# Kernel optimization log

Hardware: AMD Instinct MI355X
Metric: run time of the kernel (lower is better)

Reference implementation:

```python
import jax, jax.numpy as jnp
import numpy as np

B, T, D, H, STRIDE, MLP = 2, 2048, 1024, 16, 8, 4096
HD = D // H
EPS = 1e-5


def _ln(x, g, b):
    m = x.mean(-1, keepdims=True)
    v = x.var(-1, keepdims=True)
    return (x - m) * jax.lax.rsqrt(v + EPS) * g + b


def setup_inputs() -> dict:
    key = jax.random.key(0)
    ks = jax.random.split(key, 6)
    s = lambda k, shape: (jax.random.normal(k, shape, jnp.float32) * 0.02)
    return {
        "x": jax.random.normal(ks[0], (B, T, D), jnp.float32),
        "w_in": s(ks[1], (3 * D, D)),   # torch in_proj_weight
        "b_in": jnp.zeros((3 * D,), jnp.float32),
        "w_out": s(ks[2], (D, D)),      # attn out_proj
        "b_out": jnp.zeros((D,), jnp.float32),
        "w1": s(ks[3], (MLP, D)),       # mlp first Linear (torch layout [out,in])
        "b1": jnp.zeros((MLP,), jnp.float32),
        "w2": s(ks[4], (D, MLP)),       # mlp second Linear
        "b2": jnp.zeros((D,), jnp.float32),
        "ln1_g": jnp.ones((D,), jnp.float32),
        "ln1_b": jnp.zeros((D,), jnp.float32),
        "ln2_g": jnp.ones((D,), jnp.float32),
        "ln2_b": jnp.zeros((D,), jnp.float32),
    }


def reference(x, w_in, b_in, w_out, b_out, w1, b1, w2, b2,
              ln1_g, ln1_b, ln2_g, ln2_b):
    Bs, Ts, Ds = x.shape
    xn = _ln(x, ln1_g, ln1_b)
    # fused qkv projection (torch Linear: y = x @ W.T + b)
    qkv = xn @ w_in.T + b_in                              # [B,T,3D]
    q, k, v = jnp.split(qkv, 3, axis=-1)
    to_heads = lambda t: t.reshape(Bs, Ts, H, HD).transpose(0, 2, 1, 3)
    q, k, v = to_heads(q), to_heads(k), to_heads(v)       # [B,H,T,hd]
    scores = jnp.einsum("bhqd,bhkd->bhqk", q, k) / jnp.sqrt(jnp.float32(HD))
    # mask: rows at multiples of STRIDE attend everywhere; others only to self
    idx = jnp.arange(Ts)
    allowed = ((idx % STRIDE) == 0)[:, None] | (idx[:, None] == idx[None, :])
    scores = jnp.where(allowed, scores, -jnp.inf)
    attn = jax.nn.softmax(scores, axis=-1)
    o = jnp.einsum("bhqk,bhkd->bhqd", attn, v)            # [B,H,T,hd]
    o = o.transpose(0, 2, 1, 3).reshape(Bs, Ts, Ds)
    o = o @ w_out.T + b_out
    x = x + o
    xn = _ln(x, ln2_g, ln2_b)
    h = jax.nn.gelu(xn @ w1.T + b1, approximate=False)    # torch nn.GELU default = exact
    x = x + (h @ w2.T + b2)
    return x
```

## Files before the change

### kernel.cpp

```cpp
#include <hip/hip_runtime.h>

#define D_ 1024
#define T_ 2048
#define B_ 2
#define H_ 16
#define MLP_ 4096
#define NTOK (B_*T_)
#define QG 256
#define L2E 1.44269504088896340736f

typedef float f32x4 __attribute__((ext_vector_type(4)));
typedef __bf16 bf16x8 __attribute__((ext_vector_type(8)));

__device__ __forceinline__ unsigned short f2bf(float f) {
  unsigned int u = __float_as_uint(f);
  u += 0x7fff + ((u >> 16) & 1);
  return (unsigned short)(u >> 16);
}

__device__ __forceinline__ float wave_sum(float v) {
  for (int o = 32; o > 0; o >>= 1) v += __shfl_down(v, o, 64);
  return v;
}

__device__ __forceinline__ void gload16(const unsigned short* g, unsigned short* l) {
  __builtin_amdgcn_global_load_lds(
      (const __attribute__((address_space(1))) void*)g,
      (__attribute__((address_space(3))) void*)l, 16, 0, 0);
}

#define N4_WIN  786432
#define N4_WOUT 262144
#define N4_W1   1048576
#define N4_W2   1048576
__global__ void cast_all_kernel(const float* __restrict__ w_in,
                                const float* __restrict__ w_out,
                                const float* __restrict__ w1,
                                const float* __restrict__ w2,
                                unsigned short* __restrict__ o_in,
                                unsigned short* __restrict__ o_out,
                                unsigned short* __restrict__ o1,
                                unsigned short* __restrict__ o2) {
  int i = blockIdx.x * 256 + threadIdx.x;
  const float* src; unsigned short* dst; int j = i;
  if (i < N4_WIN) { src = w_in; dst = o_in; }
  else if ((j -= N4_WIN) < N4_WOUT) { src = w_out; dst = o_out; }
  else if ((j -= N4_WOUT) < N4_W1) { src = w1; dst = o1; }
  else { j -= N4_W1; src = w2; dst = o2; }
  float4 v = ((const float4*)src)[j];
  ushort4 o;
  o.x = f2bf(v.x); o.y = f2bf(v.y); o.z = f2bf(v.z); o.w = f2bf(v.w);
  ((ushort4*)dst)[j] = o;
}

__global__ void ln_kernel(const float* __restrict__ x, const float* __restrict__ g,
                          const float* __restrict__ b, unsigned short* __restrict__ out) {
  int row = blockIdx.x;
  int tid = threadIdx.x;
  int wave = tid >> 6, lane = tid & 63;
  float4 v = ((const float4*)(x + (size_t)row * D_))[tid];
  float s  = v.x + v.y + v.z + v.w;
  float s2 = v.x*v.x + v.y*v.y + v.z*v.z + v.w*v.w;
  s = wave_sum(s); s2 = wave_sum(s2);
  __shared__ float r1[4], r2[4];
  if (lane == 0) { r1[wave] = s; r2[wave] = s2; }
  __syncthreads();
  float ts  = r1[0] + r1[1] + r1[2] + r1[3];
  float ts2 = r2[0] + r2[1] + r2[2] + r2[3];
  float mean = ts * (1.0f / D_);
  float var  = ts2 * (1.0f / D_) - mean * mean;
  float rs = rsqrtf(var + 1e-5f);
  float4 gv = ((const float4*)g)[tid];
  float4 bv = ((const float4*)b)[tid];
  ushort4 o;
  o.x = f2bf((v.x - mean) * rs * gv.x + bv.x);
  o.y = f2bf((v.y - mean) * rs * gv.y + bv.y);
  o.z = f2bf((v.z - mean) * rs * gv.z + bv.z);
  o.w = f2bf((v.w - mean) * rs * gv.w + bv.w);
  ((ushort4*)(out + (size_t)row * D_))[tid] = o;
}

__global__ void reduce_ln_kernel(const float* __restrict__ part,
                                 const float* __restrict__ x,
                                 const float* __restrict__ bias,
                                 const float* __restrict__ g,
                                 const float* __restrict__ b,
                                 float* __restrict__ x1,
                                 unsigned short* __restrict__ xn2) {
  int row = blockIdx.x;
  int tid = threadIdx.x;
  int wave = tid >> 6, lane = tid & 63;
  size_t base = (size_t)row * (D_ / 4) + tid;
  float4 v = ((const float4*)x)[base];
  float4 bo = ((const float4*)bias)[tid];
  v.x += bo.x; v.y += bo.y; v.z += bo.z; v.w += bo.w;
#pragma unroll
  for (int c = 0; c < 2; ++c) {
    float4 p = ((const float4*)part)[(size_t)c * (NTOK * (D_ / 4)) + base];
    v.x += p.x; v.y += p.y; v.z += p.z; v.w += p.w;
  }
  ((float4*)x1)[base] = v;
  float s  = v.x + v.y + v.z + v.w;
  float s2 = v.x*v.x + v.y*v.y + v.z*v.z + v.w*v.w;
  s = wave_sum(s); s2 = wave_sum(s2);
  __shared__ float r1[4], r2[4];
  if (lane == 0) { r1[wave] = s; r2[wave] = s2; }
  __syncthreads();
  float ts  = r1[0] + r1[1] + r1[2] + r1[3];
  float ts2 = r2[0] + r2[1] + r2[2] + r2[3];
  float mean = ts * (1.0f / D_);
  float var  = ts2 * (1.0f / D_) - mean * mean;
  float rs = rsqrtf(var + 1e-5f);
  float4 gv = ((const float4*)g)[tid];
  float4 bv = ((const float4*)b)[tid];
  ushort4 o;
  o.x = f2bf((v.x - mean) * rs * gv.x + bv.x);
  o.y = f2bf((v.y - mean) * rs * gv.y + bv.y);
  o.z = f2bf((v.z - mean) * rs * gv.z + bv.z);
  o.w = f2bf((v.w - mean) * rs * gv.w + bv.w);
  ((ushort4*)xn2)[base] = o;
}

__global__ void reduce_out_kernel(const float* __restrict__ part,
                                  const float* __restrict__ x1,
                                  const float* __restrict__ bias,
                                  float* __restrict__ out) {
  int i = blockIdx.x * 256 + threadIdx.x;
  float4 v = ((const float4*)x1)[i];
  float4 bo = ((const float4*)bias)[i & (D_ / 4 - 1)];
  v.x += bo.x; v.y += bo.y; v.z += bo.z; v.w += bo.w;
#pragma unroll
  for (int c = 0; c < 2; ++c) {
    float4 p = ((const float4*)part)[(size_t)c * (NTOK * (D_ / 4)) + i];
    v.x += p.x; v.y += p.y; v.z += p.z; v.w += p.w;
  }
  ((float4*)out)[i] = v;
}

template<int EPI, int SWIZ, int LDA, int LDB, int LDC>
__global__ __launch_bounds__(256)
void gemm_kernel(const unsigned short* __restrict__ A, size_t sA,
                 const unsigned short* __restrict__ Bm, size_t sB,
                 void* __restrict__ Cv, size_t sC,
                 const float* __restrict__ bias,
                 unsigned short* __restrict__ aux1,
                 unsigned short* __restrict__ aux2,
                 int K, int nx, int ny, int kshift) {
  __shared__ __align__(16) unsigned short As[128 * 64];
  __shared__ __align__(16) unsigned short Bs[128 * 64];
  const int flat = blockIdx.x;
  int bx, by;
  if (SWIZ == 1) {
    bx = flat / ny; by = flat - bx * ny;
  } else {
    const int sxc = nx >> 1;
    const int nSuper = sxc * (ny >> 2);
    int s = flat % nSuper, pos = flat / nSuper;
    int sx = s % sxc, sy = s / sxc;
    bx = sx * 2 + (pos & 1);
    by = sy * 4 + (pos >> 1);
  }
  const int bz = blockIdx.z;
  const int batch = bz >> kshift;
  const int kOff  = (bz & ((1 << kshift) - 1)) * K;
  const int m0 = by * 128;
  const int n0 = bx * 128;
  const int tid = threadIdx.x;
  const int lane = tid & 63, wave = tid >> 6;
  const int wm = (wave >> 1) * 64, wn = (wave & 1) * 64;
  const int fr = lane & 15, q = lane >> 4;
  const int f0 = ((q)     ^ (fr & 7)) << 3;
  const int f1 = ((4 + q) ^ (fr & 7)) << 3;

  const unsigned short* aP[4];
  const unsigned short* bP[4];
  unsigned short* dA[4];
  unsigned short* dB[4];
#pragma unroll
  for (int p = 0; p < 4; ++p) {
    int l = p * 256 + tid;
    int r = l >> 3;
    int cg = (l & 7) ^ (r & 7);
    aP[p] = A  + (size_t)batch * sA + kOff + (size_t)(m0 + r) * LDA + cg * 8;
    bP[p] = Bm + (size_t)batch * sB + kOff + (size_t)(n0 + r) * LDB + cg * 8;
    dA[p] = &As[l * 8];
    dB[p] = &Bs[l * 8];
  }

  f32x4 acc[4][4] = {};
  for (int ko = 0; ko < K; ko += 64) {
    __syncthreads();
#pragma unroll
    for (int p = 0; p < 4; ++p) {
      gload16(aP[p], dA[p]); gload16(bP[p], dB[p]);
      aP[p] += 64; bP[p] += 64;
    }
    __syncthreads();
    {
      bf16x8 af[4], bfr[4];
#pragma unroll
      for (int i = 0; i < 4; ++i) af[i]  = *(const bf16x8*)&As[(wm + i * 16 + fr) * 64 + f0];
#pragma unroll
      for (int j = 0; j < 4; ++j) bfr[j] = *(const bf16x8*)&Bs[(wn + j * 16 + fr) * 64 + f0];
#pragma unroll
      for (int i = 0; i < 4; ++i)
#pragma unroll
        for (int j = 0; j < 4; ++j)
          acc[i][j] = __builtin_amdgcn_mfma_f32_16x16x32_bf16(af[i], bfr[j], acc[i][j], 0, 0, 0);
    }
    {
      bf16x8 af[4], bfr[4];
#pragma unroll
      for (int i = 0; i < 4; ++i) af[i]  = *(const bf16x8*)&As[(wm + i * 16 + fr) * 64 + f1];
#pragma unroll
      for (int j = 0; j < 4; ++j) bfr[j] = *(const bf16x8*)&Bs[(wn + j * 16 + fr) * 64 + f1];
#pragma unroll
      for (int i = 0; i < 4; ++i)
#pragma unroll
        for (int j = 0; j < 4; ++j)
          acc[i][j] = __builtin_amdgcn_mfma_f32_16x16x32_bf16(af[i], bfr[j], acc[i][j], 0, 0, 0);
    }
  }

  const int col = lane & 15, rbase = (lane >> 4) * 4;
#pragma unroll
  for (int i = 0; i < 4; ++i) {
#pragma unroll
    for (int j = 0; j < 4; ++j) {
      int gn = n0 + wn + j * 16 + col;
      int gmb = m0 + wm + i * 16 + rbase;
      float bv = (EPI == 2 || EPI == 8) ? bias[gn] : 0.0f;
#pragma unroll
      for (int r = 0; r < 4; ++r) {
        int gm = gmb + r;
        float v = acc[i][j][r] + bv;
        if (EPI == 2) {
          float u = v * (1.5957691216f + 0.0713548162f * v * v);
          float gl = v / (1.0f + exp2f(-L2E * u));
          ((unsigned short*)Cv)[(size_t)gm * LDC + gn] = f2bf(gl);
        } else if (EPI == 7) {
          ((float*)Cv)[(size_t)bz * sC + (size_t)gm * LDC + gn] = v;
        } else if (EPI == 8) {
          int sec = gn >> 10;
          int hh = (gn >> 6) & (H_ - 1);
          int dd = gn & 63;
          int t = gm & (T_ - 1);
          int b = gm >> 11;
          unsigned short bf = f2bf(v);
          if (sec == 0) {
            if (!(t & 7))
              aux1[(((size_t)(b * H_ + hh)) * QG + (t >> 3)) * 64 + dd] = bf;
          } else if (sec == 1) {
            aux2[(((size_t)(b * H_ + hh)) * T_ + t) * 64 + dd] = bf;
          } else {
            ((unsigned short*)Cv)[(size_t)gm * D_ + (gn - 2 * D_)] = bf;
          }
        }
      }
    }
  }
}

__global__ void vtrans_kernel(const unsigned short* __restrict__ vcomp,
                              unsigned short* __restrict__ Vt) {
  int blk = blockIdx.x;
  int tchunk = blk & 31;
  int bh = blk >> 5;
  int h = bh & (H_ - 1), b = bh >> 4;
  int t0 = tchunk * 64;
  __shared__ unsigned short ls[64][66];
  int tid = threadIdx.x;
#pragma unroll
  for (int it = 0; it < 16; ++it) {
    int linear = it * 256 + tid;
    int d = linear & 63, tl = linear >> 6;
    ls[d][tl] = vcomp[((size_t)(b * T_ + t0 + tl)) * D_ + h * 64 + d];
  }
  __syncthreads();
#pragma unroll
  for (int it = 0; it < 16; ++it) {
    int linear = it * 256 + tid;
    int tl = linear & 63, d = linear >> 6;
    Vt[((size_t)(bh * 64 + d)) * T_ + t0 + tl] = ls[d][tl];
  }
}

__global__ __launch_bounds__(256)
void flash_kernel(const unsigned short* __restrict__ Qg,
                  const unsigned short* __restrict__ Kh,
                  const unsigned short* __restrict__ Vt,
                  float* __restrict__ Opart,
                  float* __restrict__ ml) {
  const int kc = blockIdx.x, qt = blockIdx.y, bh = blockIdx.z;
  const int tid = threadIdx.x;
  const int lane = tid & 63, w = tid >> 6;
  const int fr = lane & 15, quad = lane >> 4;

  __shared__ __align__(16) unsigned short Qs[64 * 64];
  __shared__ __align__(16) unsigned short Ks[128 * 64];
  __shared__ __align__(16) unsigned short Vs[64 * 128];
  __shared__ __align__(16) unsigned short Ps[4 * 16 * 128];

  const unsigned short* Qbase = Qg + ((size_t)bh * 256 + qt * 64) * 64;
#pragma unroll
  for (int p = 0; p < 2; ++p) {
    int linear = p * 256 + tid;
    int r = linear >> 3, c = linear & 7;
    gload16(Qbase + r * 64 + (c ^ (r & 7)) * 8, &Qs[linear * 8]);
  }

  float m_run[4], l_run[4];
  f32x4 O[4] = {};
#pragma unroll
  for (int r = 0; r < 4; ++r) { m_run[r] = -3.0e38f; l_run[r] = 0.f; }

  const unsigned short* Kc = Kh + ((size_t)bh * T_ + kc * 512) * 64;
  const unsigned short* Vc = Vt + (size_t)bh * 64 * T_ + kc * 512;
  unsigned short* Pw = &Ps[w * 2048];
  const int arow = w * 16 + fr;

  for (int kt = 0; kt < 4; ++kt) {
    __syncthreads();
#pragma unroll
    for (int p = 0; p < 4; ++p) {
      int linear = p * 256 + tid;
      int r = linear >> 3, c = linear & 7;
      gload16(Kc + (size_t)(kt * 128 + r) * 64 + (c ^ (r & 7)) * 8, &Ks[linear * 8]);
    }
#pragma unroll
    for (int p = 0; p < 4; ++p) {
      int linear = p * 256 + tid;
      int r = linear >> 4, c = linear & 15;
      gload16(Vc + (size_t)r * T_ + kt * 128 + (c ^ (r & 7)) * 8, &Vs[linear * 8]);
    }
    __syncthreads();

    f32x4 s[8] = {};
    bf16x8 aq[2];
#pragma unroll
    for (int ks = 0; ks < 2; ++ks)
      aq[ks] = *(const bf16x8*)&Qs[arow * 64 + ((ks * 4 + quad) ^ (fr & 7)) * 8];
#pragma unroll
    for (int nf = 0; nf < 8; ++nf) {
      int krow = nf * 16 + fr;
#pragma unroll
      for (int ks = 0; ks < 2; ++ks) {
        bf16x8 bk = *(const bf16x8*)&Ks[krow * 64 + ((ks * 4 + quad) ^ (fr & 7)) * 8];
        s[nf] = __builtin_amdgcn_mfma_f32_16x16x32_bf16(aq[ks], bk, s[nf], 0, 0, 0);
      }
    }
    float alpha[4], rowsum[4];
#pragma unroll
    for (int r = 0; r < 4; ++r) {
      float mt = -3.0e38f;
#pragma unroll
      for (int nf = 0; nf < 8; ++nf) { s[nf][r] *= 0.125f; mt = fmaxf(mt, s[nf][r]); }
#pragma unroll
      for (int x = 1; x < 16; x <<= 1) mt = fmaxf(mt, __shfl_xor(mt, x, 64));
      float mn = fmaxf(m_run[r], mt);
      alpha[r] = exp2f((m_run[r] - mn) * L2E);
      m_run[r] = mn;
      rowsum[r] = 0.f;
    }
#pragma unroll
    for (int nf = 0; nf < 8; ++nf)
#pragma unroll
      for (int r = 0; r < 4; ++r) {
        float p = exp2f((s[nf][r] - m_run[r]) * L2E);
        s[nf][r] = p; rowsum[r] += p;
      }
#pragma unroll
    for (int r = 0; r < 4; ++r) {
#pragma unroll
      for (int x = 1; x < 16; x <<= 1) rowsum[r] += __shfl_xor(rowsum[r], x, 64);
      l_run[r] = l_run[r] * alpha[r] + rowsum[r];
    }
#pragma unroll
    for (int nf = 0; nf < 8; ++nf)
#pragma unroll
      for (int r = 0; r < 4; ++r) {
        int m = quad * 4 + r;
        int c = nf * 2 + (fr >> 3);
        Pw[m * 128 + ((c ^ (m & 7)) * 8) + (fr & 7)] = f2bf(s[nf][r]);
      }
#pragma unroll
    for (int nf2 = 0; nf2 < 4; ++nf2)
#pragma unroll
      for (int r = 0; r < 4; ++r) O[nf2][r] *= alpha[r];
#pragma unroll
    for (int ks2 = 0; ks2 < 4; ++ks2) {
      bf16x8 ap = *(const bf16x8*)&Pw[fr * 128 + (((ks2 * 4 + quad) ^ (fr & 7)) * 8)];
#pragma unroll
      for (int nf2 = 0; nf2 < 4; ++nf2) {
        int vrow = nf2 * 16 + fr;
        bf16x8 bv = *(const bf16x8*)&Vs[vrow * 128 + (((ks2 * 4 + quad) ^ (fr & 7)) * 8)];
        O[nf2] = __builtin_amdgcn_mfma_f32_16x16x32_bf16(ap, bv, O[nf2], 0, 0, 0);
      }
    }
  }

  int qbase = qt * 64 + w * 16;
  float* Ob = Opart + (((size_t)bh * 4 + kc) * 256 + qbase) * 64;
#pragma unroll
  for (int nf2 = 0; nf2 < 4; ++nf2)
#pragma unroll
    for (int r = 0; r < 4; ++r)
      Ob[(size_t)(quad * 4 + r) * 64 + nf2 * 16 + fr] = O[nf2][r];
  if (fr == 0) {
#pragma unroll
    for (int r = 0; r < 4; ++r) {
      size_t mi = ((((size_t)bh * 4 + kc) * 256) + qbase + quad * 4 + r) * 2;
      ml[mi] = m_run[r]; ml[mi + 1] = l_run[r];
    }
  }
}

__global__ void combine_kernel(const float* __restrict__ Opart,
                               const float* __restrict__ ml,
                               unsigned short* __restrict__ vcomp) {
  int idx = blockIdx.x * 256 + threadIdx.x;
  int c = idx & (D_ - 1);
  int qi = (idx >> 10) & (QG - 1);
  int b = idx >> 18;
  int h = c >> 6, d = c & 63;
  int bh = b * H_ + h;
  float m[4], l[4];
  float M = -3.0e38f;
#pragma unroll
  for (int ch = 0; ch < 4; ++ch) {
    size_t r = ((size_t)bh * 4 + ch) * 256 + qi;
    m[ch] = ml[r * 2]; l[ch] = ml[r * 2 + 1];
    M = fmaxf(M, m[ch]);
  }
  float osum = 0.f, lsum = 0.f;
#pragma unroll
  for (int ch = 0; ch < 4; ++ch) {
    size_t r = ((size_t)bh * 4 + ch) * 256 + qi;
    float wgt = exp2f((m[ch] - M) * L2E);
    osum += wgt * Opart[r * 64 + d];
    lsum += wgt * l[ch];
  }
  vcomp[((size_t)(b * T_ + qi * 8)) * D_ + c] = f2bf(osum / lsum);
}

extern "C" void kernel_launch(void* const* d_in, const int* in_sizes, int n_in,
                              void* d_out, int out_size, void* d_ws, size_t ws_size,
                              hipStream_t stream) {
  const float* x     = (const float*)d_in[0];
  const float* w_in  = (const float*)d_in[1];
  const float* b_in  = (const float*)d_in[2];
  const float* w_out = (const float*)d_in[3];
  const float* b_out = (const float*)d_in[4];
  const float* w1    = (const float*)d_in[5];
  const float* b1    = (const float*)d_in[6];
  const float* w2    = (const float*)d_in[7];
  const float* b2    = (const float*)d_in[8];
  const float* ln1_g = (const float*)d_in[9];
  const float* ln1_b = (const float*)d_in[10];
  const float* ln2_g = (const float*)d_in[11];
  const float* ln2_b = (const float*)d_in[12];
  float* out = (float*)d_out;

  char* ws = (char*)d_ws;
  size_t off = 0;
  auto alloc = [&](size_t bytes) -> void* {
    void* p = ws + off;
    off += (bytes + 255) & ~(size_t)255;
    return p;
  };
  unsigned short* xn    = (unsigned short*)alloc((size_t)NTOK * D_ * 2);
  unsigned short* vcomp = (unsigned short*)alloc((size_t)NTOK * D_ * 2);
  unsigned short* w_inb = (unsigned short*)alloc((size_t)3 * D_ * D_ * 2);
  unsigned short* w_outb= (unsigned short*)alloc((size_t)D_ * D_ * 2);
  unsigned short* w1b   = (unsigned short*)alloc((size_t)MLP_ * D_ * 2);
  unsigned short* w2b   = (unsigned short*)alloc((size_t)D_ * MLP_ * 2);
  unsigned short* Qg    = (unsigned short*)alloc((size_t)B_ * H_ * QG * 64 * 2);
  unsigned short* Kh    = (unsigned short*)alloc((size_t)B_ * H_ * T_ * 64 * 2);
  unsigned short* Vt    = (unsigned short*)alloc((size_t)B_ * H_ * 64 * T_ * 2);
  float*          Opart = (float*)         alloc((size_t)B_ * H_ * 4 * QG * 64 * 4);
  float*          mlbuf = (float*)         alloc((size_t)B_ * H_ * 4 * QG * 2 * 4);
  float*          x1    = (float*)         alloc((size_t)NTOK * D_ * 4);
  unsigned short* xn2   = (unsigned short*)alloc((size_t)NTOK * D_ * 2);
  unsigned short* h     = (unsigned short*)alloc((size_t)NTOK * MLP_ * 2);
  float*          P2    = (float*)         alloc((size_t)2 * NTOK * D_ * 4);

  cast_all_kernel<<<(N4_WIN + N4_WOUT + N4_W1 + N4_W2) / 256, 256, 0, stream>>>(
      w_in, w_out, w1, w2, w_inb, w_outb, w1b, w2b);

  ln_kernel<<<NTOK, 256, 0, stream>>>(x, ln1_g, ln1_b, xn);

  gemm_kernel<8, 2, D_, D_, 3 * D_><<<dim3(24 * 32, 1, 1), 256, 0, stream>>>(
      xn, 0, w_inb, 0, vcomp, 0, b_in, Qg, Kh, D_, 24, 32, 0);

  vtrans_kernel<<<1024, 256, 0, stream>>>(vcomp, Vt);

  flash_kernel<<<dim3(4, 4, 32), 256, 0, stream>>>(Qg, Kh, Vt, Opart, mlbuf);

  combine_kernel<<<2048, 256, 0, stream>>>(Opart, mlbuf, vcomp);

  gemm_kernel<7, 1, D_, D_, D_><<<dim3(8 * 32, 1, 2), 256, 0, stream>>>(
      vcomp, 0, w_outb, 0, P2, (size_t)NTOK * D_, nullptr, nullptr, nullptr,
      512, 8, 32, 1);

  reduce_ln_kernel<<<NTOK, 256, 0, stream>>>(P2, x, b_out, ln2_g, ln2_b, x1, xn2);

  gemm_kernel<2, 2, D_, D_, MLP_><<<dim3(32 * 32, 1, 1), 256, 0, stream>>>(
      xn2, 0, w1b, 0, h, 0, b1, nullptr, nullptr, D_, 32, 32, 0);

  gemm_kernel<7, 1, MLP_, MLP_, D_><<<dim3(8 * 32, 1, 2), 256, 0, stream>>>(
      h, 0, w2b, 0, P2, (size_t)NTOK * D_, nullptr, nullptr, nullptr,
      2048, 8, 32, 1);

  reduce_out_kernel<<<4096, 256, 0, stream>>>(P2, x1, b2, out);
}
```

Before: 334.1 us.

## Add 256x256 double-buffered 8-wave GEMM for MLP layers with 4-way split-K

Adds a new 512-thread GEMM kernel with 256x256 output tiles, an LDS double buffer with XOR swizzle, interleaved MFMA phases with barriers and setprio, and an XCD-aware block remap. It replaces both MLP GEMMs: the first with a GELU epilogue, the second with 4-way split-K, and the final reduction now sums four partials. The larger tiles are meant to raise operand reuse and overlap global loads with MFMA work. The workspace is restructured to alias the attention buffers with the enlarged partial-sum buffer. In exchange, fewer workgroups run per GEMM and extra partial traffic must be reduced.

Measured after the change: 332.5 us. Within noise of the previous version (-0.5%).

```diff
diff --git a/kernel.cpp b/kernel.cpp
--- a/kernel.cpp
+++ b/kernel.cpp
@@ -130,7 +130,7 @@
   float4 bo = ((const float4*)bias)[i & (D_ / 4 - 1)];
   v.x += bo.x; v.y += bo.y; v.z += bo.z; v.w += bo.w;
 #pragma unroll
-  for (int c = 0; c < 2; ++c) {
+  for (int c = 0; c < 4; ++c) {
     float4 p = ((const float4*)part)[(size_t)c * (NTOK * (D_ / 4)) + i];
     v.x += p.x; v.y += p.y; v.z += p.z; v.w += p.w;
   }
@@ -261,6 +261,195 @@
   }
 }
 
+template<int EPI>
+__global__ __launch_bounds__(512)
+void gemm256_kernel(const unsigned short* __restrict__ A, int LDA,
+                    const unsigned short* __restrict__ Bm, int LDB,
+                    void* __restrict__ Cv, size_t sC, int LDC,
+                    const float* __restrict__ bias, int K, int nxs) {
+  __shared__ __align__(16) unsigned short As[2 * 16384];
+  __shared__ __align__(16) unsigned short Bs[2 * 16384];
+  const int tid = threadIdx.x;
+  const int lane = tid & 63, w = tid >> 6;
+  const int wm = w >> 2, wn = w & 3;
+  const int fr = lane & 15, q = lane >> 4, xr = fr & 7;
+
+  const int nwg = gridDim.x;
+  const int bid = blockIdx.x;
+  const int l = (bid & 7) * (nwg >> 3) + (bid >> 3);
+  const int bx = l & ((1 << nxs) - 1), by = l >> nxs;
+  const int m0 = by * 256, n0 = bx * 256;
+  const int kOff = blockIdx.z * K;
+
+  const unsigned short* aS[4];
+  const unsigned short* bS[4];
+#pragma unroll
+  for (int s = 0; s < 4; ++s) {
+    int ls = s * 512 + tid;
+    int r = ls >> 3;
+    int cg = (ls & 7) ^ (r & 7);
+    aS[s] = A  + (size_t)(m0 + r) * LDA + kOff + cg * 8;
+    bS[s] = Bm + (size_t)(n0 + r) * LDB + kOff + cg * 8;
+  }
+  const int NT = K >> 6;
+
+#pragma unroll
+  for (int s = 0; s < 4; ++s) {
+    gload16(aS[s], &As[s * 4096 + tid * 8]);
+    gload16(bS[s], &Bs[s * 4096 + tid * 8]);
+  }
+#pragma unroll
+  for (int s = 0; s < 4; ++s) {
+    gload16(aS[s] + 64, &As[16384 + s * 4096 + tid * 8]);
+    gload16(bS[s] + 64, &Bs[16384 + s * 4096 + tid * 8]);
+  }
+  asm volatile("s_waitcnt vmcnt(8)");
+  __builtin_amdgcn_sched_barrier(0);
+  __builtin_amdgcn_s_barrier();
+  __builtin_amdgcn_sched_barrier(0);
+
+  const int aOff = ((wm * 128 + fr) << 7) + ((q ^ xr) << 4);
+  const int bOff = ((wn * 64 + fr) << 7) + ((q ^ xr) << 4);
+
+  f32x4 acc[8][4] = {};
+
+  for (int t = 0; t < NT; ++t) {
+    const int cb = (t & 1) << 15;
+    const char* Ab = (const char*)As + cb;
+    const char* Bb = (const char*)Bs + cb;
+    unsigned short* Ad = (unsigned short*)((char*)As + cb);
+    unsigned short* Bd = (unsigned short*)((char*)Bs + cb);
+    const int ko2 = (t + 2) << 6;
+    bf16x8 af[2][4], bfr[2][4];
+
+#pragma unroll
+    for (int i = 0; i < 4; ++i) {
+      af[0][i] = *(const bf16x8*)(Ab + aOff + i * 2048);
+      af[1][i] = *(const bf16x8*)(Ab + (aOff ^ 64) + i * 2048);
+    }
+#pragma unroll
+    for (int j = 0; j < 2; ++j) {
+      bfr[0][j] = *(const bf16x8*)(Bb + bOff + j * 2048);
+      bfr[1][j] = *(const bf16x8*)(Bb + (bOff ^ 64) + j * 2048);
+    }
+    __builtin_amdgcn_sched_barrier(0);
+    __builtin_amdgcn_s_barrier();
+    __builtin_amdgcn_sched_barrier(0);
+    __builtin_amdgcn_s_setprio(1);
+#pragma unroll
+    for (int i = 0; i < 4; ++i)
+#pragma unroll
+      for (int j = 0; j < 2; ++j) {
+        acc[i][j] = __builtin_amdgcn_mfma_f32_16x16x32_bf16(af[0][i], bfr[0][j], acc[i][j], 0, 0, 0);
+        acc[i][j] = __builtin_amdgcn_mfma_f32_16x16x32_bf16(af[1][i], bfr[1][j], acc[i][j], 0, 0, 0);
+      }
+    __builtin_amdgcn_s_setprio(0);
+    __builtin_amdgcn_sched_barrier(0);
+    __builtin_amdgcn_s_barrier();
+    __builtin_amdgcn_sched_barrier(0);
+
+#pragma unroll
+    for (int j = 2; j < 4; ++j) {
+      bfr[0][j] = *(const bf16x8*)(Bb + bOff + j * 2048);
+      bfr[1][j] = *(const bf16x8*)(Bb + (bOff ^ 64) + j * 2048);
+    }
+    if (t + 2 < NT) {
+      gload16(aS[0] + ko2, Ad + tid * 8);
+      gload16(aS[2] + ko2, Ad + 2 * 4096 + tid * 8);
+    }
+    __builtin_amdgcn_sched_barrier(0);
+    __builtin_amdgcn_s_barrier();
+    __builtin_amdgcn_sched_barrier(0);
+    __builtin_amdgcn_s_setprio(1);
+#pragma unroll
+    for (int i = 0; i < 4; ++i)
+#pragma unroll
+      for (int j = 0; j < 2; ++j) {
+        acc[i][2 + j] = __builtin_amdgcn_mfma_f32_16x16x32_bf16(af[0][i], bfr[0][2 + j], acc[i][2 + j], 0, 0, 0);
+        acc[i][2 + j] = __builtin_amdgcn_mfma_f32_16x16x32_bf16(af[1][i], bfr[1][2 + j], acc[i][2 + j], 0, 0, 0);
+      }
+    __builtin_amdgcn_s_setprio(0);
+    __builtin_amdgcn_sched_barrier(0);
+    __builtin_amdgcn_s_barrier();
+    __builtin_amdgcn_sched_barrier(0);
+
+#pragma unroll
+    for (int i = 0; i < 4; ++i) {
+      af[0][i] = *(const bf16x8*)(Ab + (aOff + 8192) + i * 2048);
+      af[1][i] = *(const bf16x8*)(Ab + ((aOff + 8192) ^ 64) + i * 2048);
+    }
+    if (t + 2 < NT) {
+      gload16(bS[0] + ko2, Bd + tid * 8);
+      gload16(bS[1] + ko2, Bd + 4096 + tid * 8);
+      gload16(bS[2] + ko2, Bd + 2 * 4096 + tid * 8);
+      gload16(bS[3] + ko2, Bd + 3 * 4096 + tid * 8);
+    }
+    __builtin_amdgcn_sched_barrier(0);
+    __builtin_amdgcn_s_barrier();
+    __builtin_amdgcn_sched_barrier(0);
+    __builtin_amdgcn_s_setprio(1);
+#pragma unroll
+    for (int i = 0; i < 4; ++i)
+#pragma unroll
+      for (int j = 0; j < 2; ++j) {
+        acc[4 + i][j] = __builtin_amdgcn_mfma_f32_16x16x32_bf16(af[0][i], bfr[0][j], acc[4 + i][j], 0, 0, 0);
+        acc[4 + i][j] = __builtin_amdgcn_mfma_f32_16x16x32_bf16(af[1][i], bfr[1][j], acc[4 + i][j], 0, 0, 0);
+      }
+    __builtin_amdgcn_s_setprio(0);
+    __builtin_amdgcn_sched_barrier(0);
+    __builtin_amdgcn_s_barrier();
+    __builtin_amdgcn_sched_barrier(0);
+
+    if (t + 2 < NT) {
+      gload16(aS[1] + ko2, Ad + 4096 + tid * 8);
+      gload16(aS[3] + ko2, Ad + 3 * 4096 + tid * 8);
+    }
+    if (t + 1 < NT) {
+      if (t + 2 < NT) asm volatile("s_waitcnt vmcnt(8)");
+      else            asm volatile("s_waitcnt vmcnt(0)");
+    }
+    __builtin_amdgcn_sched_barrier(0);
+    __builtin_amdgcn_s_barrier();
+    __builtin_amdgcn_sched_barrier(0);
+    __builtin_amdgcn_s_setprio(1);
+#pragma unroll
+    for (int i = 0; i < 4; ++i)
+#pragma unroll
+      for (int j = 0; j < 2; ++j) {
+        acc[4 + i][2 + j] = __builtin_amdgcn_mfma_f32_16x16x32_bf16(af[0][i], bfr[0][2 + j], acc[4 + i][2 + j], 0, 0, 0);
+        acc[4 + i][2 + j] = __builtin_amdgcn_mfma_f32_16x16x32_bf16(af[1][i], bfr[1][2 + j], acc[4 + i][2 + j], 0, 0, 0);
+      }
+    __builtin_amdgcn_s_setprio(0);
+    __builtin_amdgcn_sched_barrier(0);
+    __builtin_amdgcn_s_barrier();
+    __builtin_amdgcn_sched_barrier(0);
+  }
+
+  const int col = lane & 15, rbase = (lane >> 4) * 4;
+  const int gm0 = m0 + wm * 128 + rbase;
+  const int gn0 = n0 + wn * 64 + col;
+#pragma unroll
+  for (int mi = 0; mi < 8; ++mi) {
+#pragma unroll
+    for (int j = 0; j < 4; ++j) {
+      int gn = gn0 + j * 16;
+      float bv = (EPI == 2) ? bias[gn] : 0.0f;
+#pragma unroll
+      for (int r = 0; r < 4; ++r) {
+        int gm = gm0 + mi * 16 + r;
+        float v = acc[mi][j][r] + bv;
+        if (EPI == 2) {
+          float u = v * (1.5957691216f + 0.0713548162f * v * v);
+          float gl = v / (1.0f + exp2f(-L2E * u));
+          ((unsigned short*)Cv)[(size_t)gm * LDC + gn] = f2bf(gl);
+        } else {
+          ((float*)Cv)[(size_t)blockIdx.z * sC + (size_t)gm * LDC + gn] = v;
+        }
+      }
+    }
+  }
+}
+
 __global__ void vtrans_kernel(const unsigned short* __restrict__ vcomp,
                               unsigned short* __restrict__ Vt) {
   int blk = blockIdx.x;
@@ -468,21 +657,22 @@
     off += (bytes + 255) & ~(size_t)255;
     return p;
   };
-  unsigned short* xn    = (unsigned short*)alloc((size_t)NTOK * D_ * 2);
-  unsigned short* vcomp = (unsigned short*)alloc((size_t)NTOK * D_ * 2);
   unsigned short* w_inb = (unsigned short*)alloc((size_t)3 * D_ * D_ * 2);
   unsigned short* w_outb= (unsigned short*)alloc((size_t)D_ * D_ * 2);
   unsigned short* w1b   = (unsigned short*)alloc((size_t)MLP_ * D_ * 2);
   unsigned short* w2b   = (unsigned short*)alloc((size_t)D_ * MLP_ * 2);
-  unsigned short* Qg    = (unsigned short*)alloc((size_t)B_ * H_ * QG * 64 * 2);
-  unsigned short* Kh    = (unsigned short*)alloc((size_t)B_ * H_ * T_ * 64 * 2);
-  unsigned short* Vt    = (unsigned short*)alloc((size_t)B_ * H_ * 64 * T_ * 2);
-  float*          Opart = (float*)         alloc((size_t)B_ * H_ * 4 * QG * 64 * 4);
-  float*          mlbuf = (float*)         alloc((size_t)B_ * H_ * 4 * QG * 2 * 4);
+  unsigned short* vcomp = (unsigned short*)alloc((size_t)NTOK * D_ * 2);
   float*          x1    = (float*)         alloc((size_t)NTOK * D_ * 4);
   unsigned short* xn2   = (unsigned short*)alloc((size_t)NTOK * D_ * 2);
   unsigned short* h     = (unsigned short*)alloc((size_t)NTOK * MLP_ * 2);
-  float*          P2    = (float*)         alloc((size_t)2 * NTOK * D_ * 4);
+  char* U = (char*)alloc((size_t)4 * NTOK * D_ * 4);
+  float*          P2    = (float*)U;
+  unsigned short* xn    = (unsigned short*)U;
+  unsigned short* Qg    = (unsigned short*)(U + 8388608);
+  unsigned short* Kh    = (unsigned short*)(U + 12582912);
+  unsigned short* Vt    = (unsigned short*)(U + 20971520);
+  float*          Opart = (float*)         (U + 29360128);
+  float*          mlbuf = (float*)         (U + 37748736);
 
   cast_all_kernel<<<(N4_WIN + N4_WOUT + N4_W1 + N4_W2) / 256, 256, 0, stream>>>(
       w_in, w_out, w1, w2, w_inb, w_outb, w1b, w2b);
@@ -504,12 +694,11 @@
 
   reduce_ln_kernel<<<NTOK, 256, 0, stream>>>(P2, x, b_out, ln2_g, ln2_b, x1, xn2);
 
-  gemm_kernel<2, 2, D_, D_, MLP_><<<dim3(32 * 32, 1, 1), 256, 0, stream>>>(
-      xn2, 0, w1b, 0, h, 0, b1, nullptr, nullptr, D_, 32, 32, 0);
-
-  gemm_kernel<7, 1, MLP_, MLP_, D_><<<dim3(8 * 32, 1, 2), 256, 0, stream>>>(
-      h, 0, w2b, 0, P2, (size_t)NTOK * D_, nullptr, nullptr, nullptr,
-      2048, 8, 32, 1);
+  gemm256_kernel<2><<<dim3(256, 1, 1), 512, 0, stream>>>(
+      xn2, D_, w1b, D_, h, 0, MLP_, b1, D_, 4);
+
+  gemm256_kernel<7><<<dim3(64, 1, 4), 512, 0, stream>>>(
+      h, MLP_, w2b, MLP_, P2, (size_t)NTOK * D_, D_, nullptr, 1024, 2);
 
   reduce_out_kernel<<<4096, 256, 0, stream>>>(P2, x1, b2, out);
 }
```

## Double-buffer GEMM LDS tiles with async prefetch two stages ahead and alias workspace buffers

Applied to the files above, without the earlier changes.

Reworks the bf16 MFMA GEMM into a double-buffered pipeline: two K-tiles are preloaded into LDS, and each iteration issues loads for tile t+2 while waiting with a partial vmcnt only for tile t+1. This targets the global-load latency that was exposed between the two syncthreads in each iteration. The change also switches every GEMM to the supertile swizzle and passes leading dimensions at runtime instead of as template parameters. LDS use doubles, which may lower occupancy. Workspace buffers with disjoint lifetimes (xn, Q/K/V, partials, P2) are aliased into one region to cut the memory footprint.

After: 339.6 us. Within noise of the previous version (+1.7%).

```diff
diff --git a/kernel.cpp b/kernel.cpp
--- a/kernel.cpp
+++ b/kernel.cpp
@@ -137,34 +137,26 @@
   ((float4*)out)[i] = v;
 }
 
-template<int EPI, int SWIZ, int LDA, int LDB, int LDC>
+template<int EPI>
 __global__ __launch_bounds__(256)
-void gemm_kernel(const unsigned short* __restrict__ A, size_t sA,
-                 const unsigned short* __restrict__ Bm, size_t sB,
-                 void* __restrict__ Cv, size_t sC,
-                 const float* __restrict__ bias,
-                 unsigned short* __restrict__ aux1,
-                 unsigned short* __restrict__ aux2,
-                 int K, int nx, int ny, int kshift) {
-  __shared__ __align__(16) unsigned short As[128 * 64];
-  __shared__ __align__(16) unsigned short Bs[128 * 64];
+void gemm128p_kernel(const unsigned short* __restrict__ A, int LDA,
+                     const unsigned short* __restrict__ Bm, int LDB,
+                     void* __restrict__ Cv, size_t sC, int LDC,
+                     const float* __restrict__ bias,
+                     unsigned short* __restrict__ aux1,
+                     unsigned short* __restrict__ aux2,
+                     int K, int nx, int ny) {
+  __shared__ __align__(16) unsigned short As[2 * 8192];
+  __shared__ __align__(16) unsigned short Bs[2 * 8192];
   const int flat = blockIdx.x;
-  int bx, by;
-  if (SWIZ == 1) {
-    bx = flat / ny; by = flat - bx * ny;
-  } else {
-    const int sxc = nx >> 1;
-    const int nSuper = sxc * (ny >> 2);
-    int s = flat % nSuper, pos = flat / nSuper;
-    int sx = s % sxc, sy = s / sxc;
-    bx = sx * 2 + (pos & 1);
-    by = sy * 4 + (pos >> 1);
-  }
-  const int bz = blockIdx.z;
-  const int batch = bz >> kshift;
-  const int kOff  = (bz & ((1 << kshift) - 1)) * K;
-  const int m0 = by * 128;
-  const int n0 = bx * 128;
+  const int sxc = nx >> 1;
+  const int nSuper = sxc * (ny >> 2);
+  int s = flat % nSuper, pos = flat / nSuper;
+  int sx = s % sxc, sy = s / sxc;
+  const int bx = sx * 2 + (pos & 1);
+  const int by = sy * 4 + (pos >> 1);
+  const int m0 = by * 128, n0 = bx * 128;
+  const int kOff = blockIdx.z * K;
   const int tid = threadIdx.x;
   const int lane = tid & 63, wave = tid >> 6;
   const int wm = (wave >> 1) * 64, wn = (wave & 1) * 64;
@@ -172,36 +164,46 @@
   const int f0 = ((q)     ^ (fr & 7)) << 3;
   const int f1 = ((4 + q) ^ (fr & 7)) << 3;
 
-  const unsigned short* aP[4];
-  const unsigned short* bP[4];
-  unsigned short* dA[4];
-  unsigned short* dB[4];
+  const unsigned short* aS[4];
+  const unsigned short* bS[4];
 #pragma unroll
   for (int p = 0; p < 4; ++p) {
     int l = p * 256 + tid;
     int r = l >> 3;
     int cg = (l & 7) ^ (r & 7);
-    aP[p] = A  + (size_t)batch * sA + kOff + (size_t)(m0 + r) * LDA + cg * 8;
-    bP[p] = Bm + (size_t)batch * sB + kOff + (size_t)(n0 + r) * LDB + cg * 8;
-    dA[p] = &As[l * 8];
-    dB[p] = &Bs[l * 8];
-  }
+    aS[p] = A  + (size_t)(m0 + r) * LDA + kOff + cg * 8;
+    bS[p] = Bm + (size_t)(n0 + r) * LDB + kOff + cg * 8;
+  }
+  const int NT = K >> 6;
+
+#pragma unroll
+  for (int p = 0; p < 4; ++p) {
+    gload16(aS[p], &As[p * 2048 + tid * 8]);
+    gload16(bS[p], &Bs[p * 2048 + tid * 8]);
+  }
+#pragma unroll
+  for (int p = 0; p < 4; ++p) {
+    gload16(aS[p] + 64, &As[8192 + p * 2048 + tid * 8]);
+    gload16(bS[p] + 64, &Bs[8192 + p * 2048 + tid * 8]);
+  }
+  asm volatile("s_waitcnt vmcnt(8)");
+  __builtin_amdgcn_sched_barrier(0);
+  __builtin_amdgcn_s_barrier();
 
   f32x4 acc[4][4] = {};
-  for (int ko = 0; ko < K; ko += 64) {
-    __syncthreads();
-#pragma unroll
-    for (int p = 0; p < 4; ++p) {
-      gload16(aP[p], dA[p]); gload16(bP[p], dB[p]);
-      aP[p] += 64; bP[p] += 64;
-    }
-    __syncthreads();
+  for (int t = 0; t < NT; ++t) {
+    const int cb = (t & 1) << 13;
+    const unsigned short* Ab = As + cb;
+    const unsigned short* Bb = Bs + cb;
+    unsigned short* Ad = As + cb;
+    unsigned short* Bd = Bs + cb;
+    const int ko2 = (t + 2) << 6;
     {
       bf16x8 af[4], bfr[4];
 #pragma unroll
-      for (int i = 0; i < 4; ++i) af[i]  = *(const bf16x8*)&As[(wm + i * 16 + fr) * 64 + f0];
-#pragma unroll
-      for (int j = 0; j < 4; ++j) bfr[j] = *(const bf16x8*)&Bs[(wn + j * 16 + fr) * 64 + f0];
+      for (int i = 0; i < 4; ++i) af[i]  = *(const bf16x8*)&Ab[(wm + i * 16 + fr) * 64 + f0];
+#pragma unroll
+      for (int j = 0; j < 4; ++j) bfr[j] = *(const bf16x8*)&Bb[(wn + j * 16 + fr) * 64 + f0];
 #pragma unroll
       for (int i = 0; i < 4; ++i)
 #pragma unroll
@@ -211,15 +213,29 @@
     {
       bf16x8 af[4], bfr[4];
 #pragma unroll
-      for (int i = 0; i < 4; ++i) af[i]  = *(const bf16x8*)&As[(wm + i * 16 + fr) * 64 + f1];
-#pragma unroll
-      for (int j = 0; j < 4; ++j) bfr[j] = *(const bf16x8*)&Bs[(wn + j * 16 + fr) * 64 + f1];
+      for (int i = 0; i < 4; ++i) af[i]  = *(const bf16x8*)&Ab[(wm + i * 16 + fr) * 64 + f1];
+#pragma unroll
+      for (int j = 0; j < 4; ++j) bfr[j] = *(const bf16x8*)&Bb[(wn + j * 16 + fr) * 64 + f1];
 #pragma unroll
       for (int i = 0; i < 4; ++i)
 #pragma unroll
         for (int j = 0; j < 4; ++j)
           acc[i][j] = __builtin_amdgcn_mfma_f32_16x16x32_bf16(af[i], bfr[j], acc[i][j], 0, 0, 0);
     }
+    __builtin_amdgcn_s_barrier();
+    if (t + 2 < NT) {
+#pragma unroll
+      for (int p = 0; p < 4; ++p) {
+        gload16(aS[p] + ko2, Ad + p * 2048 + tid * 8);
+        gload16(bS[p] + ko2, Bd + p * 2048 + tid * 8);
+      }
+    }
+    if (t + 1 < NT) {
+      if (t + 2 < NT) asm volatile("s_waitcnt vmcnt(8)");
+      else            asm volatile("s_waitcnt vmcnt(0)");
+      __builtin_amdgcn_sched_barrier(0);
+    }
+    __builtin_amdgcn_s_barrier();
   }
 
   const int col = lane & 15, rbase = (lane >> 4) * 4;
@@ -239,8 +255,8 @@
           float gl = v / (1.0f + exp2f(-L2E * u));
           ((unsigned short*)Cv)[(size_t)gm * LDC + gn] = f2bf(gl);
         } else if (EPI == 7) {
-          ((float*)Cv)[(size_t)bz * sC + (size_t)gm * LDC + gn] = v;
-        } else if (EPI == 8) {
+          ((float*)Cv)[(size_t)blockIdx.z * sC + (size_t)gm * LDC + gn] = v;
+        } else {
           int sec = gn >> 10;
           int hh = (gn >> 6) & (H_ - 1);
           int dd = gn & 63;
@@ -468,29 +484,30 @@
     off += (bytes + 255) & ~(size_t)255;
     return p;
   };
-  unsigned short* xn    = (unsigned short*)alloc((size_t)NTOK * D_ * 2);
-  unsigned short* vcomp = (unsigned short*)alloc((size_t)NTOK * D_ * 2);
   unsigned short* w_inb = (unsigned short*)alloc((size_t)3 * D_ * D_ * 2);
   unsigned short* w_outb= (unsigned short*)alloc((size_t)D_ * D_ * 2);
   unsigned short* w1b   = (unsigned short*)alloc((size_t)MLP_ * D_ * 2);
   unsigned short* w2b   = (unsigned short*)alloc((size_t)D_ * MLP_ * 2);
-  unsigned short* Qg    = (unsigned short*)alloc((size_t)B_ * H_ * QG * 64 * 2);
-  unsigned short* Kh    = (unsigned short*)alloc((size_t)B_ * H_ * T_ * 64 * 2);
-  unsigned short* Vt    = (unsigned short*)alloc((size_t)B_ * H_ * 64 * T_ * 2);
-  float*          Opart = (float*)         alloc((size_t)B_ * H_ * 4 * QG * 64 * 4);
-  float*          mlbuf = (float*)         alloc((size_t)B_ * H_ * 4 * QG * 2 * 4);
+  unsigned short* vcomp = (unsigned short*)alloc((size_t)NTOK * D_ * 2);
   float*          x1    = (float*)         alloc((size_t)NTOK * D_ * 4);
   unsigned short* xn2   = (unsigned short*)alloc((size_t)NTOK * D_ * 2);
   unsigned short* h     = (unsigned short*)alloc((size_t)NTOK * MLP_ * 2);
-  float*          P2    = (float*)         alloc((size_t)2 * NTOK * D_ * 4);
+  char* U = (char*)alloc((size_t)40 * 1024 * 1024);
+  float*          P2    = (float*)U;
+  unsigned short* xn    = (unsigned short*)U;
+  unsigned short* Qg    = (unsigned short*)(U + 8388608);
+  unsigned short* Kh    = (unsigned short*)(U + 12582912);
+  unsigned short* Vt    = (unsigned short*)(U + 20971520);
+  float*          Opart = (float*)         (U + 29360128);
+  float*          mlbuf = (float*)         (U + 37748736);
 
   cast_all_kernel<<<(N4_WIN + N4_WOUT + N4_W1 + N4_W2) / 256, 256, 0, stream>>>(
       w_in, w_out, w1, w2, w_inb, w_outb, w1b, w2b);
 
   ln_kernel<<<NTOK, 256, 0, stream>>>(x, ln1_g, ln1_b, xn);
 
-  gemm_kernel<8, 2, D_, D_, 3 * D_><<<dim3(24 * 32, 1, 1), 256, 0, stream>>>(
-      xn, 0, w_inb, 0, vcomp, 0, b_in, Qg, Kh, D_, 24, 32, 0);
+  gemm128p_kernel<8><<<dim3(24 * 32, 1, 1), 256, 0, stream>>>(
+      xn, D_, w_inb, D_, vcomp, 0, 3 * D_, b_in, Qg, Kh, 1024, 24, 32);
 
   vtrans_kernel<<<1024, 256, 0, stream>>>(vcomp, Vt);
 
@@ -498,18 +515,18 @@
 
   combine_kernel<<<2048, 256, 0, stream>>>(Opart, mlbuf, vcomp);
 
-  gemm_kernel<7, 1, D_, D_, D_><<<dim3(8 * 32, 1, 2), 256, 0, stream>>>(
-      vcomp, 0, w_outb, 0, P2, (size_t)NTOK * D_, nullptr, nullptr, nullptr,
-      512, 8, 32, 1);
+  gemm128p_kernel<7><<<dim3(8 * 32, 1, 2), 256, 0, stream>>>(
+      vcomp, D_, w_outb, D_, P2, (size_t)NTOK * D_, D_, nullptr, nullptr, nullptr,
+      512, 8, 32);
 
   reduce_ln_kernel<<<NTOK, 256, 0, stream>>>(P2, x, b_out, ln2_g, ln2_b, x1, xn2);
 
-  gemm_kernel<2, 2, D_, D_, MLP_><<<dim3(32 * 32, 1, 1), 256, 0, stream>>>(
-      xn2, 0, w1b, 0, h, 0, b1, nullptr, nullptr, D_, 32, 32, 0);
-
-  gemm_kernel<7, 1, MLP_, MLP_, D_><<<dim3(8 * 32, 1, 2), 256, 0, stream>>>(
-      h, 0, w2b, 0, P2, (size_t)NTOK * D_, nullptr, nullptr, nullptr,
-      2048, 8, 32, 1);
+  gemm128p_kernel<2><<<dim3(32 * 32, 1, 1), 256, 0, stream>>>(
+      xn2, D_, w1b, D_, h, 0, MLP_, b1, nullptr, nullptr, 1024, 32, 32);
+
+  gemm128p_kernel<7><<<dim3(8 * 32, 1, 2), 256, 0, stream>>>(
+      h, MLP_, w2b, MLP_, P2, (size_t)NTOK * D_, D_, nullptr, nullptr, nullptr,
+      2048, 8, 32);
 
   reduce_out_kernel<<<4096, 256, 0, stream>>>(P2, x1, b2, out);
 }
```
